# Kernel optimization log

Hardware: AMD Instinct MI355X
Metric: run time of the kernel (lower is better)

## Reference

```python
import jax, jax.numpy as jnp
import numpy as np

D_MODEL = 1024
D_STATE = 16
D_CONV = 4
EXPAND = 2
E = EXPAND * D_MODEL  # 2048
B, L = 4, 4096


def setup_inputs() -> dict:
    key = jax.random.key(0)
    ks = jax.random.split(key, 8)
    x = jax.random.normal(ks[0], (B, L, D_MODEL), dtype=jnp.float32)
    W_in = jax.random.normal(ks[1], (D_MODEL, 2 * E), dtype=jnp.float32) * 0.02
    b_in = jnp.zeros((2 * E,), dtype=jnp.float32)
    conv_w = jax.random.normal(ks[2], (E, 1, D_CONV), dtype=jnp.float32) * 0.1
    conv_b = jnp.zeros((E,), dtype=jnp.float32)
    A = jax.random.normal(ks[3], (E, D_STATE), dtype=jnp.float32) * 0.01
    C = jax.random.normal(ks[4], (E, D_STATE), dtype=jnp.float32) * 0.01
    Dp = jnp.ones((E,), dtype=jnp.float32) * 0.01
    W_out = jax.random.normal(ks[5], (E, D_MODEL), dtype=jnp.float32) * 0.02
    b_out = jnp.zeros((D_MODEL,), dtype=jnp.float32)
    return {"x": x, "W_in": W_in, "b_in": b_in, "conv_w": conv_w,
            "conv_b": conv_b, "A": A, "C": C, "Dp": Dp,
            "W_out": W_out, "b_out": b_out}


def reference(x, W_in, b_in, conv_w, conv_b, A, C, Dp, W_out, b_out):
    Bb, Ll, _ = x.shape
    # in_proj then split into x_proj / z  (each [B, L, E])
    x_and_z = x @ W_in + b_in
    x_proj, z = jnp.split(x_and_z, 2, axis=-1)
    # causal depthwise conv1d: torch padding=d_conv-1 then truncate to L
    xc = jnp.transpose(x_proj, (0, 2, 1))  # [B, E, L]
    xc = jax.lax.conv_general_dilated(
        xc, conv_w, window_strides=(1,), padding=[(D_CONV - 1, 0)],
        dimension_numbers=("NCH", "OIH", "NCH"), feature_group_count=E)
    x_conv = jnp.transpose(xc + conv_b[None, :, None], (0, 2, 1))  # [B, L, E]

    # sequential SSM scan: h_t = tanh(x_t @ A + h_{t-1}); y_t = h_t @ C^T + D*x_t
    def step(h, xt):
        h = jnp.tanh(xt @ A + h)          # [B, d_state]
        yt = h @ C.T + Dp * xt            # [B, E]
        return h, yt

    h0 = jnp.zeros((Bb, D_STATE), dtype=x.dtype)
    _, ys = jax.lax.scan(step, h0, jnp.transpose(x_conv, (1, 0, 2)))  # [L, B, E]
    x_s4 = jnp.transpose(ys, (1, 0, 2))  # [B, L, E]

    y = jax.nn.sigmoid(z) * x_s4
    return y @ W_out + b_out
```

## Files before the change

### kernel.cpp

```cpp
#include <hip/hip_runtime.h>
#include <cstdint>
#include <cstddef>

#define D_MODEL 1024
#define D_STATE 16
#define E_DIM   2048
#define SEQ     4096
#define M_ROWS  16384

typedef unsigned short u16;
typedef unsigned int   u32;
typedef __attribute__((ext_vector_type(8))) short short8;
typedef __attribute__((ext_vector_type(4))) float f32x4;

__device__ __forceinline__ u16 f2bf(float f) {
    u32 u = __float_as_uint(f);
    u32 r = (u + 0x7fffu + ((u >> 16) & 1u)) >> 16;
    return (u16)r;
}
__device__ __forceinline__ float bf2f(u16 h) {
    return __uint_as_float(((u32)h) << 16);
}

#define BM 128
#define BN 128
#define HC_STR 17

__device__ __forceinline__ size_t xcp_off(int m, int n) {
    int Mt = m >> 7, mr = m & 127;
    int Kt = n >> 6, nt = n & 63;
    int c16 = nt >> 3;
    int c = (mr >> 4) * 128 + (c16 >> 2) * 64 + (c16 & 3) * 16 + (mr & 15);
    return ((size_t)Mt * 32 + Kt) * 8192 + (size_t)c * 8 + (nt & 7);
}

template <int MODE>
__global__ __launch_bounds__(256)
void mfma_gemm(const u16* __restrict__ Ag, const u16* __restrict__ Bg,
               int K, int Nst,
               const float* __restrict__ bias,
               u16* __restrict__ outb, float* __restrict__ outf,
               const float* __restrict__ Hm, const float* __restrict__ Cm,
               const float* __restrict__ Dp, u16* __restrict__ XCp)
{
    const int t     = threadIdx.x;
    const int lane  = t & 63;
    const int w     = t >> 6;
    const int col_l = lane & 15;
    const int quad  = lane >> 4;
    const int wm = (w & 1) * 64;
    const int wn = (w >> 1) * 64;

    const int L = blockIdx.y * gridDim.x + blockIdx.x;
    const int xcd = L & 7, g = L >> 3;
    const int ntile = g % gridDim.x;
    const int mtile = xcd * (gridDim.y >> 3) + g / gridDim.x;
    const int bm = mtile * BM;
    const int bn = ntile * BN;

    const int KT = K >> 6;
    const u16* aw = Ag + (size_t)mtile * KT * 8192 + (size_t)(w & 1) * 4096
                       + (size_t)lane * 8;
    const u16* bw = Bg + (size_t)ntile * KT * 8192 + (size_t)(w >> 1) * 4096
                       + (size_t)lane * 8;

    f32x4 acc[4][4] = {};

    auto ldfrag = [&](short8* da, short8* db, size_t off, int step) {
#pragma unroll
        for (int i = 0; i < 4; ++i) {
            da[i] = *(const short8*)(aw + off + (size_t)((i * 2 + step) * 512));
            db[i] = *(const short8*)(bw + off + (size_t)((i * 2 + step) * 512));
        }
    };
    auto mfma16 = [&](short8* af, short8* bfr) {
#pragma unroll
        for (int i = 0; i < 4; ++i)
#pragma unroll
            for (int j = 0; j < 4; ++j)
                acc[i][j] = __builtin_amdgcn_mfma_f32_16x16x32_bf16(
                    af[i], bfr[j], acc[i][j], 0, 0, 0);
    };

    short8 A0[4], B0[4], A1[4], B1[4];
    size_t off = 0;
    ldfrag(A0, B0, 0, 0);
    ldfrag(A1, B1, 0, 1);
    for (int kt = 0; kt < KT; ++kt) {
        mfma16(A0, B0);
        if (kt + 1 < KT) ldfrag(A0, B0, off + 8192, 0);
        mfma16(A1, B1);
        if (kt + 1 < KT) ldfrag(A1, B1, off + 8192, 1);
        off += 8192;
    }

    if (MODE == 0) {
#pragma unroll
        for (int j = 0; j < 4; ++j) {
            int n = bn + wn + j * 16 + col_l;
            float bv = bias[n];
#pragma unroll
            for (int i = 0; i < 4; ++i) {
                int mb = bm + wm + i * 16 + quad * 4;
#pragma unroll
                for (int p = 0; p < 4; ++p)
                    outb[(size_t)(mb + p) * Nst + n] = f2bf(acc[i][j][p] + bv);
            }
        }
    } else if (MODE == 1) {
        __shared__ float Hs[BM * HC_STR];
        __shared__ float Cs[BN * HC_STR];
        for (int idx = t; idx < BM * D_STATE; idx += 256)
            Hs[(idx >> 4) * HC_STR + (idx & 15)] =
                Hm[(size_t)(bm + (idx >> 4)) * D_STATE + (idx & 15)];
        for (int idx = t; idx < BN * D_STATE; idx += 256)
            Cs[(idx >> 4) * HC_STR + (idx & 15)] =
                Cm[(size_t)(bn + (idx >> 4)) * D_STATE + (idx & 15)];
        __syncthreads();
#pragma unroll
        for (int i = 0; i < 4; ++i) {
            int ml = wm + i * 16 + quad * 4;
#pragma unroll
            for (int p = 0; p < 4; ++p) {
                float hrow[D_STATE];
#pragma unroll
                for (int s = 0; s < D_STATE; ++s)
                    hrow[s] = Hs[(ml + p) * HC_STR + s];
#pragma unroll
                for (int j = 0; j < 4; ++j) {
                    int nl = wn + j * 16 + col_l;
                    int n = bn + nl;
                    float z = acc[i][j][p] + bias[n];
                    float sig = 1.f / (1.f + __expf(-z));
                    float dot = 0.f;
#pragma unroll
                    for (int s = 0; s < D_STATE; ++s)
                        dot += hrow[s] * Cs[nl * HC_STR + s];
                    size_t offx = xcp_off(bm + ml + p, n);
                    float xc = bf2f(XCp[offx]);
                    XCp[offx] = f2bf(sig * (dot + Dp[n] * xc));
                }
            }
        }
    } else {
#pragma unroll
        for (int j = 0; j < 4; ++j) {
            int n = bn + wn + j * 16 + col_l;
            float bv = bias[n];
#pragma unroll
            for (int i = 0; i < 4; ++i) {
                int mb = bm + wm + i * 16 + quad * 4;
#pragma unroll
                for (int p = 0; p < 4; ++p)
                    outf[(size_t)(mb + p) * Nst + n] = acc[i][j][p] + bv;
            }
        }
    }
}

__global__ __launch_bounds__(256)
void pack_x_kernel(const float* __restrict__ x, u16* __restrict__ xp)
{
    const int Kt = blockIdx.x;
    const int Mt = blockIdx.y;
    const int t  = threadIdx.x;
    u16* dst = xp + ((size_t)Mt * 16 + Kt) * 8192;
#pragma unroll
    for (int i = 0; i < 4; ++i) {
        int c   = i * 256 + t;
        int ell = c & 63;
        int row = Mt * 128 + (c >> 7) * 16 + (ell & 15);
        int col = Kt * 64 + (((c >> 6) & 1) * 4 + (ell >> 4)) * 8;
        const float4* src = (const float4*)&x[(size_t)row * D_MODEL + col];
        float4 a = src[0], b = src[1];
        alignas(16) u16 o[8] = {f2bf(a.x), f2bf(a.y), f2bf(a.z), f2bf(a.w),
                                f2bf(b.x), f2bf(b.y), f2bf(b.z), f2bf(b.w)};
        *(short8*)(dst + c * 8) = *(const short8*)o;
    }
}

__global__ __launch_bounds__(256)
void pack_w_kernel(const float* __restrict__ W, u16* __restrict__ out,
                   int Wstride, int colOff, int KT)
{
    const int Kt = blockIdx.x;
    const int Nt = blockIdx.y;
    const int t  = threadIdx.x;
    u16* dst = out + ((size_t)Nt * KT + Kt) * 8192;
#pragma unroll
    for (int i = 0; i < 4; ++i) {
        int c    = i * 256 + t;
        int ell  = c & 63;
        int nrow = Nt * 128 + (c >> 7) * 16 + (ell & 15);
        int kcol = Kt * 64 + (((c >> 6) & 1) * 4 + (ell >> 4)) * 8;
        alignas(16) u16 o[8];
#pragma unroll
        for (int q = 0; q < 8; ++q)
            o[q] = f2bf(W[(size_t)(kcol + q) * Wstride + colOff + nrow]);
        *(short8*)(dst + c * 8) = *(const short8*)o;
    }
}

__global__ __launch_bounds__(256)
void conv_kernel(const u16* __restrict__ XP, const float* __restrict__ conv_w,
                 const float* __restrict__ conv_b, u16* __restrict__ XCp)
{
    const int Kt = blockIdx.x;
    const int Mt = blockIdx.y;
    const int t  = threadIdx.x;
    u16* dst = XCp + ((size_t)Mt * 32 + Kt) * 8192;
#pragma unroll
    for (int i = 0; i < 4; ++i) {
        int c   = i * 256 + t;
        int ell = c & 63;
        int mr  = (c >> 7) * 16 + (ell & 15);
        int e   = Kt * 64 + (((c >> 6) & 1) * 4 + (ell >> 4)) * 8;
        int m   = Mt * 128 + mr;
        int l   = m & (SEQ - 1);
        float acc[8];
        {
            float4 c0 = *(const float4*)&conv_b[e];
            float4 c1 = *(const float4*)&conv_b[e + 4];
            acc[0] = c0.x; acc[1] = c0.y; acc[2] = c0.z; acc[3] = c0.w;
            acc[4] = c1.x; acc[5] = c1.y; acc[6] = c1.z; acc[7] = c1.w;
        }
#pragma unroll
        for (int k = 0; k < 4; ++k) {
            if (l - 3 + k >= 0) {
                const short8 xv = *(const short8*)&XP[(size_t)(m - 3 + k) * E_DIM + e];
#pragma unroll
                for (int j = 0; j < 8; ++j)
                    acc[j] += bf2f((u16)xv[j]) * conv_w[(size_t)(e + j) * 4 + k];
            }
        }
        alignas(16) u16 o[8];
#pragma unroll
        for (int j = 0; j < 8; ++j) o[j] = f2bf(acc[j]);
        *(short8*)(dst + c * 8) = *(const short8*)o;
    }
}

__global__ __launch_bounds__(256)
void u_part_kernel(const u16* __restrict__ XCp, const float* __restrict__ Amat,
                   float* __restrict__ Up)
{
    const int kp = blockIdx.x;
    const int Mt = blockIdx.y;
    const int t  = threadIdx.x;
    const int rr = t >> 1;
    const int z  = t & 1;
    const int msub = rr >> 4, r = rr & 15;

    float acc[16];
#pragma unroll
    for (int s = 0; s < 16; ++s) acc[s] = 0.f;

#pragma unroll
    for (int kk = 0; kk < 2; ++kk) {
        const int Kt = kp * 2 + kk;
        const u16* tile = XCp + ((size_t)Mt * 32 + Kt) * 8192;
#pragma unroll
        for (int q = 0; q < 4; ++q) {
            const int c = msub * 128 + z * 64 + q * 16 + r;
            const short8 xv = *(const short8*)(tile + (size_t)c * 8);
            const int e0 = Kt * 64 + (z * 4 + q) * 8;
#pragma unroll
            for (int j = 0; j < 8; ++j) {
                float xq = bf2f((u16)xv[j]);
                const float4* ar = (const float4*)&Amat[(size_t)(e0 + j) * D_STATE];
#pragma unroll
                for (int s4 = 0; s4 < 4; ++s4) {
                    float4 a = ar[s4];
                    acc[s4 * 4 + 0] += xq * a.x; acc[s4 * 4 + 1] += xq * a.y;
                    acc[s4 * 4 + 2] += xq * a.z; acc[s4 * 4 + 3] += xq * a.w;
                }
            }
        }
    }
#pragma unroll
    for (int s = 0; s < 16; ++s) acc[s] += __shfl_xor(acc[s], 1);

    if (z == 0) {
        const int m = Mt * 128 + rr;
        float4* dst = (float4*)&Up[((size_t)kp * M_ROWS + m) * D_STATE];
        dst[0] = make_float4(acc[0], acc[1], acc[2], acc[3]);
        dst[1] = make_float4(acc[4], acc[5], acc[6], acc[7]);
        dst[2] = make_float4(acc[8], acc[9], acc[10], acc[11]);
        dst[3] = make_float4(acc[12], acc[13], acc[14], acc[15]);
    }
}

__global__ __launch_bounds__(256)
void u_reduce_kernel(const float* __restrict__ Up, float* __restrict__ U)
{
    const int idx = blockIdx.x * 256 + threadIdx.x;
    const float4* src = (const float4*)Up;
    float4 s = src[idx];
#pragma unroll
    for (int kp = 1; kp < 16; ++kp) {
        float4 v = src[(size_t)kp * (M_ROWS * D_STATE / 4) + idx];
        s.x += v.x; s.y += v.y; s.z += v.z; s.w += v.w;
    }
    ((float4*)U)[idx] = s;
}

__global__ __launch_bounds__(64)
void scan_kernel(const float* __restrict__ U, float* __restrict__ H)
{
    const int t = threadIdx.x;
    const int b = t >> 4;
    const int s = t & 15;
    const float* u = U + (size_t)b * SEQ * D_STATE + s;
    float*       h = H + (size_t)b * SEQ * D_STATE + s;

    float cur[8], nxt[8];
#pragma unroll
    for (int j = 0; j < 8; ++j) cur[j] = u[(size_t)j * D_STATE];

    float hv = 0.f;
    for (int l0 = 0; l0 < SEQ; l0 += 8) {
        if (l0 + 8 < SEQ) {
#pragma unroll
            for (int j = 0; j < 8; ++j)
                nxt[j] = u[(size_t)(l0 + 8 + j) * D_STATE];
        }
#pragma unroll
        for (int j = 0; j < 8; ++j) {
            float ex = __expf(2.f * (cur[j] + hv));
            hv = 1.f - 2.f / (ex + 1.f);
            h[(size_t)(l0 + j) * D_STATE] = hv;
        }
#pragma unroll
        for (int j = 0; j < 8; ++j) cur[j] = nxt[j];
    }
}

extern "C" void kernel_launch(void* const* d_in, const int* in_sizes, int n_in,
                              void* d_out, int out_size, void* d_ws, size_t ws_size,
                              hipStream_t stream)
{
    const float* x      = (const float*)d_in[0];
    const float* W_in   = (const float*)d_in[1];
    const float* b_in   = (const float*)d_in[2];
    const float* conv_w = (const float*)d_in[3];
    const float* conv_b = (const float*)d_in[4];
    const float* Amat   = (const float*)d_in[5];
    const float* Cmat   = (const float*)d_in[6];
    const float* Dp     = (const float*)d_in[7];
    const float* W_out  = (const float*)d_in[8];
    const float* b_out  = (const float*)d_in[9];
    float* out = (float*)d_out;

    char* ws = (char*)d_ws;
    u16*   xbp  = (u16*)(ws);
    u16*   Wp0  = (u16*)(ws +  33554432);
    u16*   Wp1  = (u16*)(ws +  37748736);
    u16*   Wp2  = (u16*)(ws +  41943040);
    u16*   XCp  = (u16*)(ws +  46137344);
    float* U    = (float*)(ws + 113246208);
    float* H    = (float*)(ws + 114294784);
    float* Up   = (float*)(ws + 115343360);
    u16*   XP   = (u16*)d_out;

    pack_x_kernel<<<dim3(16, 128), 256, 0, stream>>>(x, xbp);
    pack_w_kernel<<<dim3(16, 16), 256, 0, stream>>>(W_in, Wp0, 2 * E_DIM, 0, 16);
    pack_w_kernel<<<dim3(16, 16), 256, 0, stream>>>(W_in, Wp1, 2 * E_DIM, E_DIM, 16);
    pack_w_kernel<<<dim3(32, 8), 256, 0, stream>>>(W_out, Wp2, D_MODEL, 0, 32);

    mfma_gemm<0><<<dim3(16, 128), 256, 0, stream>>>(
        xbp, Wp0, D_MODEL, E_DIM, b_in, XP, nullptr, nullptr, nullptr, nullptr, nullptr);

    conv_kernel<<<dim3(32, 128), 256, 0, stream>>>(XP, conv_w, conv_b, XCp);

    u_part_kernel<<<dim3(16, 128), 256, 0, stream>>>(XCp, Amat, Up);
    u_reduce_kernel<<<256, 256, 0, stream>>>(Up, U);
    scan_kernel<<<1, 64, 0, stream>>>(U, H);

    mfma_gemm<1><<<dim3(16, 128), 256, 0, stream>>>(
        xbp, Wp1, D_MODEL, 0, b_in + E_DIM, nullptr, nullptr, H, Cmat, Dp, XCp);

    mfma_gemm<2><<<dim3(8, 128), 256, 0, stream>>>(
        XCp, Wp2, E_DIM, D_MODEL, b_out, nullptr, out, nullptr, nullptr, nullptr, nullptr);
}
```

Baseline: 1.087 ms.

## Enlarge GEMM block tile to 512x128 with 128x128 per-wave tiles

Each wave now computes a full 128x128 output tile (8x8 MFMA accumulators) instead of 64x64, and a block covers 512 rows. The grids shrink by 4x in M to match. The goal is more MFMA work per loaded fragment, which raises arithmetic intensity and cuts global and L2 fragment traffic. The cost is heavy register use: 256 accumulator floats plus 32 short8 fragments per thread, hence launch_bounds(256,1). That risks spills or low occupancy, and with far fewer blocks (512 or 256) the 256 CUs may be poorly filled.

Result: slower. 2.753 ms (+153.2%).

```diff
diff --git a/kernel.cpp b/kernel.cpp
--- a/kernel.cpp
+++ b/kernel.cpp
@@ -22,8 +22,6 @@
     return __uint_as_float(((u32)h) << 16);
 }
 
-#define BM 128
-#define BN 128
 #define HC_STR 17
 
 __device__ __forceinline__ size_t xcp_off(int m, int n) {
@@ -35,7 +33,7 @@
 }
 
 template <int MODE>
-__global__ __launch_bounds__(256)
+__global__ __launch_bounds__(256, 1)
 void mfma_gemm(const u16* __restrict__ Ag, const u16* __restrict__ Bg,
                int K, int Nst,
                const float* __restrict__ bias,
@@ -48,87 +46,84 @@
     const int w     = t >> 6;
     const int col_l = lane & 15;
     const int quad  = lane >> 4;
-    const int wm = (w & 1) * 64;
-    const int wn = (w >> 1) * 64;
 
     const int L = blockIdx.y * gridDim.x + blockIdx.x;
     const int xcd = L & 7, g = L >> 3;
-    const int ntile = g % gridDim.x;
-    const int mtile = xcd * (gridDim.y >> 3) + g / gridDim.x;
-    const int bm = mtile * BM;
-    const int bn = ntile * BN;
+    const int ntile  = g % gridDim.x;
+    const int mtileB = xcd * (gridDim.y >> 3) + g / gridDim.x;
+    const int bmB = mtileB * 512;
+    const int bm  = bmB + w * 128;
+    const int bn  = ntile * 128;
 
     const int KT = K >> 6;
-    const u16* aw = Ag + (size_t)mtile * KT * 8192 + (size_t)(w & 1) * 4096
-                       + (size_t)lane * 8;
-    const u16* bw = Bg + (size_t)ntile * KT * 8192 + (size_t)(w >> 1) * 4096
-                       + (size_t)lane * 8;
-
-    f32x4 acc[4][4] = {};
-
-    auto ldfrag = [&](short8* da, short8* db, size_t off, int step) {
-#pragma unroll
-        for (int i = 0; i < 4; ++i) {
+    const u16* aw = Ag + ((size_t)(mtileB * 4 + w) * KT) * 8192 + (size_t)lane * 8;
+    const u16* bw = Bg + (size_t)ntile * KT * 8192 + (size_t)lane * 8;
+
+    f32x4 acc[8][8] = {};
+
+    auto ldf = [&](short8* da, short8* db, size_t off, int step) {
+#pragma unroll
+        for (int i = 0; i < 8; ++i) {
             da[i] = *(const short8*)(aw + off + (size_t)((i * 2 + step) * 512));
             db[i] = *(const short8*)(bw + off + (size_t)((i * 2 + step) * 512));
         }
     };
-    auto mfma16 = [&](short8* af, short8* bfr) {
-#pragma unroll
-        for (int i = 0; i < 4; ++i)
-#pragma unroll
-            for (int j = 0; j < 4; ++j)
+    auto mm = [&](short8* a8, short8* b8) {
+#pragma unroll
+        for (int i = 0; i < 8; ++i)
+#pragma unroll
+            for (int j = 0; j < 8; ++j)
                 acc[i][j] = __builtin_amdgcn_mfma_f32_16x16x32_bf16(
-                    af[i], bfr[j], acc[i][j], 0, 0, 0);
+                    a8[i], b8[j], acc[i][j], 0, 0, 0);
     };
 
-    short8 A0[4], B0[4], A1[4], B1[4];
+    short8 A0[8], B0[8], A1[8], B1[8];
+    ldf(A0, B0, 0, 0);
+    ldf(A1, B1, 0, 1);
     size_t off = 0;
-    ldfrag(A0, B0, 0, 0);
-    ldfrag(A1, B1, 0, 1);
     for (int kt = 0; kt < KT; ++kt) {
-        mfma16(A0, B0);
-        if (kt + 1 < KT) ldfrag(A0, B0, off + 8192, 0);
-        mfma16(A1, B1);
-        if (kt + 1 < KT) ldfrag(A1, B1, off + 8192, 1);
+        const bool p = kt + 1 < KT;
+        mm(A0, B0); if (p) ldf(A0, B0, off + 8192, 0);
+        mm(A1, B1); if (p) ldf(A1, B1, off + 8192, 1);
         off += 8192;
     }
 
     if (MODE == 0) {
 #pragma unroll
-        for (int j = 0; j < 4; ++j) {
-            int n = bn + wn + j * 16 + col_l;
+        for (int j = 0; j < 8; ++j) {
+            int n = bn + j * 16 + col_l;
             float bv = bias[n];
 #pragma unroll
-            for (int i = 0; i < 4; ++i) {
-                int mb = bm + wm + i * 16 + quad * 4;
+            for (int i = 0; i < 8; ++i) {
+                int mb = bm + i * 16 + quad * 4;
 #pragma unroll
                 for (int p = 0; p < 4; ++p)
                     outb[(size_t)(mb + p) * Nst + n] = f2bf(acc[i][j][p] + bv);
             }
         }
     } else if (MODE == 1) {
-        __shared__ float Hs[BM * HC_STR];
-        __shared__ float Cs[BN * HC_STR];
-        for (int idx = t; idx < BM * D_STATE; idx += 256)
+        __shared__ float Hs[512 * HC_STR];
+        __shared__ float Cs[128 * HC_STR];
+        for (int idx = t; idx < 512 * D_STATE; idx += 256)
             Hs[(idx >> 4) * HC_STR + (idx & 15)] =
-                Hm[(size_t)(bm + (idx >> 4)) * D_STATE + (idx & 15)];
-        for (int idx = t; idx < BN * D_STATE; idx += 256)
+                Hm[((size_t)bmB + (idx >> 4)) * D_STATE + (idx & 15)];
+        for (int idx = t; idx < 128 * D_STATE; idx += 256)
             Cs[(idx >> 4) * HC_STR + (idx & 15)] =
-                Cm[(size_t)(bn + (idx >> 4)) * D_STATE + (idx & 15)];
+                Cm[((size_t)(bn + (idx >> 4))) * D_STATE + (idx & 15)];
         __syncthreads();
 #pragma unroll
-        for (int i = 0; i < 4; ++i) {
-            int ml = wm + i * 16 + quad * 4;
+        for (int i = 0; i < 8; ++i) {
+            int mlp = w * 128 + i * 16 + quad * 4;
 #pragma unroll
             for (int p = 0; p < 4; ++p) {
+                int row = mlp + p;
                 float hrow[D_STATE];
 #pragma unroll
                 for (int s = 0; s < D_STATE; ++s)
-                    hrow[s] = Hs[(ml + p) * HC_STR + s];
-#pragma unroll
-                for (int j = 0; j < 4; ++j) {
-                    int nl = wn + j * 16 + col_l;
+                    hrow[s] = Hs[row * HC_STR + s];
+#pragma unroll
+                for (int j = 0; j < 8; ++j) {
+                    int nl = j * 16 + col_l;
                     int n = bn + nl;
                     float z = acc[i][j][p] + bias[n];
                     float sig = 1.f / (1.f + __expf(-z));
@@ -136,7 +131,7 @@
 #pragma unroll
                     for (int s = 0; s < D_STATE; ++s)
                         dot += hrow[s] * Cs[nl * HC_STR + s];
-                    size_t offx = xcp_off(bm + ml + p, n);
+                    size_t offx = xcp_off(bmB + row, n);
                     float xc = bf2f(XCp[offx]);
                     XCp[offx] = f2bf(sig * (dot + Dp[n] * xc));
                 }
@@ -144,12 +139,12 @@
         }
     } else {
 #pragma unroll
-        for (int j = 0; j < 4; ++j) {
-            int n = bn + wn + j * 16 + col_l;
+        for (int j = 0; j < 8; ++j) {
+            int n = bn + j * 16 + col_l;
             float bv = bias[n];
 #pragma unroll
-            for (int i = 0; i < 4; ++i) {
-                int mb = bm + wm + i * 16 + quad * 4;
+            for (int i = 0; i < 8; ++i) {
+                int mb = bm + i * 16 + quad * 4;
 #pragma unroll
                 for (int p = 0; p < 4; ++p)
                     outf[(size_t)(mb + p) * Nst + n] = acc[i][j][p] + bv;
@@ -367,7 +362,7 @@
     pack_w_kernel<<<dim3(16, 16), 256, 0, stream>>>(W_in, Wp1, 2 * E_DIM, E_DIM, 16);
     pack_w_kernel<<<dim3(32, 8), 256, 0, stream>>>(W_out, Wp2, D_MODEL, 0, 32);
 
-    mfma_gemm<0><<<dim3(16, 128), 256, 0, stream>>>(
+    mfma_gemm<0><<<dim3(16, 32), 256, 0, stream>>>(
         xbp, Wp0, D_MODEL, E_DIM, b_in, XP, nullptr, nullptr, nullptr, nullptr, nullptr);
 
     conv_kernel<<<dim3(32, 128), 256, 0, stream>>>(XP, conv_w, conv_b, XCp);
@@ -376,9 +371,9 @@
     u_reduce_kernel<<<256, 256, 0, stream>>>(Up, U);
     scan_kernel<<<1, 64, 0, stream>>>(U, H);
 
-    mfma_gemm<1><<<dim3(16, 128), 256, 0, stream>>>(
+    mfma_gemm<1><<<dim3(16, 32), 256, 0, stream>>>(
         xbp, Wp1, D_MODEL, 0, b_in + E_DIM, nullptr, nullptr, H, Cmat, Dp, XCp);
 
-    mfma_gemm<2><<<dim3(8, 128), 256, 0, stream>>>(
+    mfma_gemm<2><<<dim3(8, 32), 256, 0, stream>>>(
         XCp, Wp2, E_DIM, D_MODEL, b_out, nullptr, out, nullptr, nullptr, nullptr, nullptr);
 }
```
